# Kernel optimization log

Measured on AMD Instinct MI355X. Metric: run time of the kernel, lower is better.

The kernel has to match this reference:

```python
import jax, jax.numpy as jnp
import numpy as np

N = 10000
E = 160000
DIMS = [512, 512, 512, 256]  # in -> hidden -> hidden -> out (num_layers=3)
EPS = 1e-12  # F.normalize default eps


def _sage_layer(x, edge_index, Wl, b, Wr):
    # PyG SAGEConv (mean aggr, normalize=True):
    # out = lin_l(mean_{j in N(i)} x_j) + lin_r(x_i), then L2-normalize rows.
    src = edge_index[0]
    dst = edge_index[1]
    msg = x[src]  # [E, d] gather of source-node features
    agg = jax.ops.segment_sum(msg, dst, num_segments=N)  # [N, d]
    cnt = jax.ops.segment_sum(jnp.ones((E,), x.dtype), dst, num_segments=N)
    mean = agg / jnp.maximum(cnt, 1.0)[:, None]
    out = mean @ Wl.T + b + x @ Wr.T
    norm = jnp.sqrt(jnp.sum(out * out, axis=-1, keepdims=True))
    return out / jnp.maximum(norm, EPS)


def setup_inputs() -> dict:
    key = jax.random.key(0)
    ks = jax.random.split(key, 2 + 3 * len(DIMS))
    x = jax.random.normal(ks[0], (N, DIMS[0]), dtype=jnp.float32)
    edge_index = jax.random.randint(ks[1], (2, E), 0, N, dtype=jnp.int64)
    inp = {"x": x, "edge_index": edge_index}
    k = 2
    for i in range(len(DIMS) - 1):
        din, dout = DIMS[i], DIMS[i + 1]
        s = 1.0 / np.sqrt(din)
        inp[f"Wl{i}"] = jax.random.uniform(ks[k], (dout, din), jnp.float32, -s, s); k += 1
        inp[f"b{i}"] = jax.random.uniform(ks[k], (dout,), jnp.float32, -s, s); k += 1
        inp[f"Wr{i}"] = jax.random.uniform(ks[k], (dout, din), jnp.float32, -s, s); k += 1
    return inp


def reference(x, edge_index, Wl0, b0, Wr0, Wl1, b1, Wr1, Wl2, b2, Wr2):
    params = [(Wl0, b0, Wr0), (Wl1, b1, Wr1), (Wl2, b2, Wr2)]
    for Wl, b, Wr in params:
        x = _sage_layer(x, edge_index, Wl, b, Wr)
        x = jax.nn.relu(x)
        # F.dropout(training=False) is identity at inference
    return x
```

## Files before the change

### kernel.cpp

```cpp
#include <hip/hip_runtime.h>

#define NN 10000

typedef __attribute__((ext_vector_type(8))) short short8;
typedef __attribute__((ext_vector_type(4))) float f32x4;

__device__ __forceinline__ ushort f2b(float f) {
    union { float f; uint32_t u; } v; v.f = f;
    uint32_t u = v.u;
    return (ushort)((u + 0x7fffu + ((u >> 16) & 1u)) >> 16);
}
__device__ __forceinline__ uint packbf(float a, float b) {
    return (uint)f2b(a) | ((uint)f2b(b) << 16);
}
__device__ __forceinline__ float blo(uint u) {
    union { uint u; float f; } v; v.u = u << 16; return v.f;
}
__device__ __forceinline__ float bhi(uint u) {
    union { uint u; float f; } v; v.u = u & 0xffff0000u; return v.f;
}

__global__ __launch_bounds__(256) void zero_int(int* __restrict__ p, int n) {
    int i = blockIdx.x * 256 + threadIdx.x;
    if (i < n) p[i] = 0;
}

__global__ __launch_bounds__(256) void count_dst(const int* __restrict__ dst,
                                                 int* __restrict__ counts, int E) {
    int i = blockIdx.x * 256 + threadIdx.x;
    if (i < E) atomicAdd(&counts[dst[i]], 1);
}

__global__ __launch_bounds__(1024) void scan_build(const int* __restrict__ counts,
                                                   int* __restrict__ offsets,
                                                   int* __restrict__ cursor,
                                                   float* __restrict__ inv_cnt, int n) {
    __shared__ int part[1024];
    int tid = threadIdx.x;
    int per = (n + 1023) / 1024;
    int base = tid * per;
    int s = 0;
    for (int i = 0; i < per; i++) { int idx = base + i; if (idx < n) s += counts[idx]; }
    part[tid] = s;
    __syncthreads();
    for (int off = 1; off < 1024; off <<= 1) {
        int v = (tid >= off) ? part[tid - off] : 0;
        __syncthreads();
        part[tid] += v;
        __syncthreads();
    }
    int run = (tid > 0) ? part[tid - 1] : 0;
    for (int i = 0; i < per; i++) {
        int idx = base + i;
        if (idx < n) {
            int c = counts[idx];
            offsets[idx] = run;
            cursor[idx]  = run;
            inv_cnt[idx] = 1.0f / fmaxf((float)c, 1.0f);
            run += c;
        }
    }
}

__global__ __launch_bounds__(256) void scatter_edges(const int* __restrict__ src,
                                                     const int* __restrict__ dst,
                                                     int* __restrict__ cursor,
                                                     int* __restrict__ sorted_src, int E) {
    int i = blockIdx.x * 256 + threadIdx.x;
    if (i < E) {
        int p = atomicAdd(&cursor[dst[i]], 1);
        sorted_src[p] = src[i];
    }
}

__global__ __launch_bounds__(256) void cvt_x(const float* __restrict__ in,
                                             ushort* __restrict__ xcat, int n4) {
    int i = blockIdx.x * 256 + threadIdx.x;
    if (i >= n4) return;
    int idx = i * 4;
    int node = idx >> 9;
    int col  = idx & 511;
    float4 v = *(const float4*)(in + (size_t)node * 512 + col);
    uint2 p;
    p.x = packbf(v.x, v.y);
    p.y = packbf(v.z, v.w);
    *(uint2*)(xcat + (size_t)node * 1024 + 512 + col) = p;
}

__global__ __launch_bounds__(256) void cvt_w_all(const float* __restrict__ Wl0,
                                                 const float* __restrict__ Wr0,
                                                 const float* __restrict__ Wl1,
                                                 const float* __restrict__ Wr1,
                                                 const float* __restrict__ Wl2,
                                                 const float* __restrict__ Wr2,
                                                 ushort* __restrict__ out, int n4) {
    int i = blockIdx.x * 256 + threadIdx.x;
    if (i >= n4) return;
    int idx = i * 4;
    int row = idx >> 10;
    int col = idx & 1023;
    const float* Wl; const float* Wr; int r;
    if (row < 512)       { Wl = Wl0; Wr = Wr0; r = row; }
    else if (row < 1024) { Wl = Wl1; Wr = Wr1; r = row - 512; }
    else                 { Wl = Wl2; Wr = Wr2; r = row - 1024; }
    const float* src = (col < 512) ? (Wl + (size_t)r * 512 + col)
                                   : (Wr + (size_t)r * 512 + col - 512);
    float4 v = *(const float4*)src;
    uint2 p;
    p.x = packbf(v.x, v.y);
    p.y = packbf(v.z, v.w);
    *(uint2*)(out + idx) = p;
}

__global__ __launch_bounds__(256) void agg_mean(ushort* __restrict__ xcat,
                                                const int* __restrict__ offsets,
                                                const int* __restrict__ counts,
                                                const int* __restrict__ sorted_src,
                                                const float* __restrict__ inv_cnt,
                                                float* __restrict__ rowss, int n) {
    if (threadIdx.x < 16) {
        int z = blockIdx.x * 16 + (int)threadIdx.x;
        if (z < n) rowss[z] = 0.f;
    }
    int wave = threadIdx.x >> 6;
    int lane = threadIdx.x & 63;
    int node = blockIdx.x * 4 + wave;
    if (node >= n) return;
    int start = offsets[node];
    int cnt   = counts[node];
    float inv = inv_cnt[node];

    const uint* xr = (const uint*)xcat + 256;
    int l4 = lane * 4;

    float acc[8];
#pragma unroll
    for (int k = 0; k < 8; k++) acc[k] = 0.f;

#define ACC8(v) do { \
    acc[0] += blo(v.x); acc[1] += bhi(v.x); \
    acc[2] += blo(v.y); acc[3] += bhi(v.y); \
    acc[4] += blo(v.z); acc[5] += bhi(v.z); \
    acc[6] += blo(v.w); acc[7] += bhi(v.w); } while (0)

    int e = 0;
    for (; e + 8 <= cnt; e += 8) {
        int s[8];
#pragma unroll
        for (int u = 0; u < 8; u++) s[u] = sorted_src[start + e + u];
        uint4 v[8];
#pragma unroll
        for (int u = 0; u < 8; u++) v[u] = *(const uint4*)(xr + (size_t)s[u] * 512 + l4);
#pragma unroll
        for (int u = 0; u < 8; u++) ACC8(v[u]);
    }
    for (; e < cnt; e++) {
        int s0 = sorted_src[start + e];
        uint4 v0 = *(const uint4*)(xr + (size_t)s0 * 512 + l4);
        ACC8(v0);
    }
#undef ACC8

    uint4 o;
    o.x = packbf(acc[0] * inv, acc[1] * inv);
    o.y = packbf(acc[2] * inv, acc[3] * inv);
    o.z = packbf(acc[4] * inv, acc[5] * inv);
    o.w = packbf(acc[6] * inv, acc[7] * inv);
    *(uint4*)(xcat + (size_t)node * 1024 + lane * 8) = o;
}

__global__ __launch_bounds__(256) void gemm_mfma(const ushort* __restrict__ A,
                                                 const ushort* __restrict__ B,
                                                 const float* __restrict__ bias,
                                                 ushort* __restrict__ Cb,
                                                 float* __restrict__ rowss,
                                                 int M, int Nn) {
    __shared__ ushort Asl[64 * 32];
    __shared__ ushort Bsl[128 * 32];
    const int tid  = threadIdx.x;
    const int w    = tid >> 6;
    const int lane = tid & 63;
    const int bm = blockIdx.y * 64, bn = blockIdx.x * 128;
    const int wm = (w & 1) * 32, wn = (w >> 1) * 64;
    const int row16 = lane & 15, q = lane >> 4;

    f32x4 acc[2][4];
#pragma unroll
    for (int i = 0; i < 2; i++)
#pragma unroll
        for (int j = 0; j < 4; j++) acc[i][j] = (f32x4){0.f, 0.f, 0.f, 0.f};

    const int sc_r = lane >> 2;
    const int sc_s = lane & 3;
    const int koff = sc_s ^ ((sc_r >> 1) & 3);
    const int swz  = (row16 >> 1) & 3;

    for (int k0 = 0; k0 < 1024; k0 += 32) {
        {
            int rloc = w * 16 + sc_r;
            int grow = bm + rloc; grow = grow < M ? grow : M - 1;
            const ushort* gp = A + (size_t)grow * 1024 + k0 + koff * 8;
            __builtin_amdgcn_global_load_lds(
                (const __attribute__((address_space(1))) uint32_t*)gp,
                (__attribute__((address_space(3))) uint32_t*)&Asl[w * 512],
                16, 0, 0);
        }
#pragma unroll
        for (int c = 0; c < 2; c++) {
            int chunk = w * 2 + c;
            int rloc  = chunk * 16 + sc_r;
            const ushort* gp = B + (size_t)(bn + rloc) * 1024 + k0 + koff * 8;
            __builtin_amdgcn_global_load_lds(
                (const __attribute__((address_space(1))) uint32_t*)gp,
                (__attribute__((address_space(3))) uint32_t*)&Bsl[chunk * 512],
                16, 0, 0);
        }
        __syncthreads();

        short8 af[2], bfr[4];
        int s = q ^ swz;
#pragma unroll
        for (int i = 0; i < 2; i++) {
            int r = wm + i * 16 + row16;
            af[i] = *(const short8*)&Asl[r * 32 + s * 8];
        }
#pragma unroll
        for (int j = 0; j < 4; j++) {
            int rn = wn + j * 16 + row16;
            bfr[j] = *(const short8*)&Bsl[rn * 32 + s * 8];
        }
#pragma unroll
        for (int i = 0; i < 2; i++)
#pragma unroll
            for (int j = 0; j < 4; j++)
                acc[i][j] = __builtin_amdgcn_mfma_f32_16x16x32_bf16(
                    af[i], bfr[j], acc[i][j], 0, 0, 0);
        __syncthreads();
    }

    float bias_v[4];
#pragma unroll
    for (int j = 0; j < 4; j++) bias_v[j] = bias[bn + wn + row16 + j * 16];

#pragma unroll
    for (int i = 0; i < 2; i++) {
#pragma unroll
        for (int r2 = 0; r2 < 4; r2++) {
            int row = bm + wm + i * 16 + q * 4 + r2;
            float v0 = acc[i][0][r2] + bias_v[0];
            float v1 = acc[i][1][r2] + bias_v[1];
            float v2 = acc[i][2][r2] + bias_v[2];
            float v3 = acc[i][3][r2] + bias_v[3];
            float ssp = v0 * v0 + v1 * v1 + v2 * v2 + v3 * v3;
            ssp += __shfl_xor(ssp, 1, 64);
            ssp += __shfl_xor(ssp, 2, 64);
            ssp += __shfl_xor(ssp, 4, 64);
            ssp += __shfl_xor(ssp, 8, 64);
            if (row < M) {
                ushort* Cp = Cb + (size_t)row * Nn + bn + wn + row16;
                Cp[0]  = f2b(v0);
                Cp[16] = f2b(v1);
                Cp[32] = f2b(v2);
                Cp[48] = f2b(v3);
                if (row16 == 0) atomicAdd(&rowss[row], ssp);
            }
        }
    }
}

template <int DOUT, bool FINAL>
__global__ __launch_bounds__(256) void apply_scale(const ushort* __restrict__ Cb,
                                                   const float* __restrict__ rowss,
                                                   ushort* __restrict__ xcat,
                                                   float* __restrict__ outf, int n) {
    int wave = threadIdx.x >> 6;
    int lane = threadIdx.x & 63;
    int node = blockIdx.x * 4 + wave;
    if (node >= n) return;
    float scale = 1.0f / fmaxf(sqrtf(rowss[node]), 1e-12f);

    if (DOUT == 512) {
        uint4 v = *(const uint4*)(Cb + (size_t)node * 512 + lane * 8);
        float r0 = fmaxf(blo(v.x) * scale, 0.f), r1 = fmaxf(bhi(v.x) * scale, 0.f);
        float r2 = fmaxf(blo(v.y) * scale, 0.f), r3 = fmaxf(bhi(v.y) * scale, 0.f);
        float r4 = fmaxf(blo(v.z) * scale, 0.f), r5 = fmaxf(bhi(v.z) * scale, 0.f);
        float r6 = fmaxf(blo(v.w) * scale, 0.f), r7 = fmaxf(bhi(v.w) * scale, 0.f);
        uint4 o;
        o.x = packbf(r0, r1); o.y = packbf(r2, r3);
        o.z = packbf(r4, r5); o.w = packbf(r6, r7);
        *(uint4*)(xcat + (size_t)node * 1024 + 512 + lane * 8) = o;
    } else {
        uint2 v = *(const uint2*)(Cb + (size_t)node * 256 + lane * 4);
        float4 o;
        o.x = fmaxf(blo(v.x) * scale, 0.f);
        o.y = fmaxf(bhi(v.x) * scale, 0.f);
        o.z = fmaxf(blo(v.y) * scale, 0.f);
        o.w = fmaxf(bhi(v.y) * scale, 0.f);
        *(float4*)(outf + (size_t)node * 256 + lane * 4) = o;
    }
}

extern "C" void kernel_launch(void* const* d_in, const int* in_sizes, int n_in,
                              void* d_out, int out_size, void* d_ws, size_t ws_size,
                              hipStream_t stream) {
    const float* x    = (const float*)d_in[0];
    const int*   edge = (const int*)d_in[1];
    const float* Wl0  = (const float*)d_in[2];
    const float* b0   = (const float*)d_in[3];
    const float* Wr0  = (const float*)d_in[4];
    const float* Wl1  = (const float*)d_in[5];
    const float* b1   = (const float*)d_in[6];
    const float* Wr1  = (const float*)d_in[7];
    const float* Wl2  = (const float*)d_in[8];
    const float* b2   = (const float*)d_in[9];
    const float* Wr2  = (const float*)d_in[10];

    const int E = in_sizes[1] / 2;

    char* ws = (char*)d_ws;
    int*    counts  = (int*)(ws + 0);
    int*    offsets = (int*)(ws + 40960);
    int*    cursor  = (int*)(ws + 81920);
    float*  invc    = (float*)(ws + 122880);
    int*    sorted  = (int*)(ws + 163840);
    ushort* Wcat    = (ushort*)(ws + 804864);
    ushort* xcat    = (ushort*)(ws + 3426304);
    ushort* Cb      = (ushort*)(ws + 23906304);
    float*  rowss   = (float*)(ws + 34146304);

    ushort* Wc0 = Wcat;
    ushort* Wc1 = Wcat + 512 * 1024;
    ushort* Wc2 = Wcat + 1024 * 1024;

    zero_int<<<(NN + 255) / 256, 256, 0, stream>>>(counts, NN);
    count_dst<<<(E + 255) / 256, 256, 0, stream>>>(edge + E, counts, E);
    scan_build<<<1, 1024, 0, stream>>>(counts, offsets, cursor, invc, NN);
    scatter_edges<<<(E + 255) / 256, 256, 0, stream>>>(edge, edge + E, cursor, sorted, E);

    cvt_x<<<(NN * 512 / 4 + 255) / 256, 256, 0, stream>>>(x, xcat, NN * 512 / 4);
    cvt_w_all<<<(1280 * 1024 / 4 + 255) / 256, 256, 0, stream>>>(
        Wl0, Wr0, Wl1, Wr1, Wl2, Wr2, Wcat, 1280 * 1024 / 4);

    const int gyM = (NN + 63) / 64;
    const int gb  = (NN + 3) / 4;

    agg_mean<<<gb, 256, 0, stream>>>(xcat, offsets, counts, sorted, invc, rowss, NN);
    gemm_mfma<<<dim3(4, gyM), 256, 0, stream>>>(xcat, Wc0, b0, Cb, rowss, NN, 512);
    apply_scale<512, false><<<gb, 256, 0, stream>>>(Cb, rowss, xcat, nullptr, NN);
    agg_mean<<<gb, 256, 0, stream>>>(xcat, offsets, counts, sorted, invc, rowss, NN);
    gemm_mfma<<<dim3(4, gyM), 256, 0, stream>>>(xcat, Wc1, b1, Cb, rowss, NN, 512);
    apply_scale<512, false><<<gb, 256, 0, stream>>>(Cb, rowss, xcat, nullptr, NN);
    agg_mean<<<gb, 256, 0, stream>>>(xcat, offsets, counts, sorted, invc, rowss, NN);
    gemm_mfma<<<dim3(2, gyM), 256, 0, stream>>>(xcat, Wc2, b2, Cb, rowss, NN, 256);
    apply_scale<256, true><<<gb, 256, 0, stream>>>(Cb, rowss, nullptr, (float*)d_out, NN);
}
```

Measured before the change: 280.5 us.

## Fuse normalize+ReLU into next-layer aggregation and widen GEMM N-tile

Removes the separate apply_scale kernels for the hidden layers. Normalization and ReLU are now applied on the fly inside a new agg_mid kernel. It reads the unnormalized bf16 GEMM output and the per-node sum of squares, using double-buffered rowss arrays. The GEMM is templated on N-tile width, so the first two layers use 256-wide tiles (half the blocks, A loaded once per pair). The trade-off is recomputing a sqrt/reciprocal per gathered edge and an extra random rowss load. Fewer GEMM blocks (2x157) may also reduce occupancy on a large GPU.

```diff
diff --git a/kernel.cpp b/kernel.cpp
--- a/kernel.cpp
+++ b/kernel.cpp
@@ -112,15 +112,15 @@
     *(uint2*)(out + idx) = p;
 }
 
-__global__ __launch_bounds__(256) void agg_mean(ushort* __restrict__ xcat,
-                                                const int* __restrict__ offsets,
-                                                const int* __restrict__ counts,
-                                                const int* __restrict__ sorted_src,
-                                                const float* __restrict__ inv_cnt,
-                                                float* __restrict__ rowss, int n) {
+__global__ __launch_bounds__(256) void agg_first(ushort* __restrict__ xcat,
+                                                 const int* __restrict__ offsets,
+                                                 const int* __restrict__ counts,
+                                                 const int* __restrict__ sorted_src,
+                                                 const float* __restrict__ inv_cnt,
+                                                 float* __restrict__ rowss_next, int n) {
     if (threadIdx.x < 16) {
         int z = blockIdx.x * 16 + (int)threadIdx.x;
-        if (z < n) rowss[z] = 0.f;
+        if (z < n) rowss_next[z] = 0.f;
     }
     int wave = threadIdx.x >> 6;
     int lane = threadIdx.x & 63;
@@ -169,24 +169,105 @@
     *(uint4*)(xcat + (size_t)node * 1024 + lane * 8) = o;
 }
 
+__global__ __launch_bounds__(256) void agg_mid(ushort* __restrict__ xcat,
+                                               const ushort* __restrict__ Cb,
+                                               const float* __restrict__ rowss_prev,
+                                               float* __restrict__ rowss_next,
+                                               const int* __restrict__ offsets,
+                                               const int* __restrict__ counts,
+                                               const int* __restrict__ sorted_src,
+                                               const float* __restrict__ inv_cnt, int n) {
+    if (threadIdx.x < 16) {
+        int z = blockIdx.x * 16 + (int)threadIdx.x;
+        if (z < n) rowss_next[z] = 0.f;
+    }
+    int wave = threadIdx.x >> 6;
+    int lane = threadIdx.x & 63;
+    int node = blockIdx.x * 4 + wave;
+    if (node >= n) return;
+    int start = offsets[node];
+    int cnt   = counts[node];
+    float inv = inv_cnt[node];
+    int l4 = lane * 4;
+
+    const uint* cb = (const uint*)Cb;
+
+    {
+        float si = 1.0f / fmaxf(sqrtf(rowss_prev[node]), 1e-12f);
+        uint4 c = *(const uint4*)(cb + (size_t)node * 256 + l4);
+        float r0 = fmaxf(blo(c.x), 0.f) * si, r1 = fmaxf(bhi(c.x), 0.f) * si;
+        float r2 = fmaxf(blo(c.y), 0.f) * si, r3 = fmaxf(bhi(c.y), 0.f) * si;
+        float r4 = fmaxf(blo(c.z), 0.f) * si, r5 = fmaxf(bhi(c.z), 0.f) * si;
+        float r6 = fmaxf(blo(c.w), 0.f) * si, r7 = fmaxf(bhi(c.w), 0.f) * si;
+        uint4 o;
+        o.x = packbf(r0, r1); o.y = packbf(r2, r3);
+        o.z = packbf(r4, r5); o.w = packbf(r6, r7);
+        *(uint4*)(xcat + (size_t)node * 1024 + 512 + lane * 8) = o;
+    }
+
+    float acc[8];
+#pragma unroll
+    for (int k = 0; k < 8; k++) acc[k] = 0.f;
+
+#define ACCS(v, sc) do { \
+    acc[0] += fmaxf(blo(v.x), 0.f) * sc; acc[1] += fmaxf(bhi(v.x), 0.f) * sc; \
+    acc[2] += fmaxf(blo(v.y), 0.f) * sc; acc[3] += fmaxf(bhi(v.y), 0.f) * sc; \
+    acc[4] += fmaxf(blo(v.z), 0.f) * sc; acc[5] += fmaxf(bhi(v.z), 0.f) * sc; \
+    acc[6] += fmaxf(blo(v.w), 0.f) * sc; acc[7] += fmaxf(bhi(v.w), 0.f) * sc; } while (0)
+
+    int e = 0;
+    for (; e + 4 <= cnt; e += 4) {
+        int s[4];
+#pragma unroll
+        for (int u = 0; u < 4; u++) s[u] = sorted_src[start + e + u];
+        float sc[4];
+#pragma unroll
+        for (int u = 0; u < 4; u++)
+            sc[u] = 1.0f / fmaxf(sqrtf(rowss_prev[s[u]]), 1e-12f);
+        uint4 v[4];
+#pragma unroll
+        for (int u = 0; u < 4; u++) v[u] = *(const uint4*)(cb + (size_t)s[u] * 256 + l4);
+#pragma unroll
+        for (int u = 0; u < 4; u++) ACCS(v[u], sc[u]);
+    }
+    for (; e < cnt; e++) {
+        int s0 = sorted_src[start + e];
+        float sc0 = 1.0f / fmaxf(sqrtf(rowss_prev[s0]), 1e-12f);
+        uint4 v0 = *(const uint4*)(cb + (size_t)s0 * 256 + l4);
+        ACCS(v0, sc0);
+    }
+#undef ACCS
+
+    uint4 o;
+    o.x = packbf(acc[0] * inv, acc[1] * inv);
+    o.y = packbf(acc[2] * inv, acc[3] * inv);
+    o.z = packbf(acc[4] * inv, acc[5] * inv);
+    o.w = packbf(acc[6] * inv, acc[7] * inv);
+    *(uint4*)(xcat + (size_t)node * 1024 + lane * 8) = o;
+}
+
+template <int BN>
 __global__ __launch_bounds__(256) void gemm_mfma(const ushort* __restrict__ A,
                                                  const ushort* __restrict__ B,
                                                  const float* __restrict__ bias,
                                                  ushort* __restrict__ Cb,
                                                  float* __restrict__ rowss,
                                                  int M, int Nn) {
+    constexpr int NWN = BN / 64;
+    constexpr int WRC = NWN;
     __shared__ ushort Asl[64 * 32];
-    __shared__ ushort Bsl[128 * 32];
+    __shared__ ushort Bsl[BN * 32];
     const int tid  = threadIdx.x;
     const int w    = tid >> 6;
     const int lane = tid & 63;
-    const int bm = blockIdx.y * 64, bn = blockIdx.x * 128;
-    const int wm = (w & 1) * 32, wn = (w >> 1) * 64;
+    const int bm = blockIdx.y * 64, bn = blockIdx.x * BN;
+    const int wn = (w % NWN) * 64;
+    const int wm = (w / NWN) * (WRC * 16);
     const int row16 = lane & 15, q = lane >> 4;
 
-    f32x4 acc[2][4];
-#pragma unroll
-    for (int i = 0; i < 2; i++)
+    f32x4 acc[WRC][4];
+#pragma unroll
+    for (int i = 0; i < WRC; i++)
 #pragma unroll
         for (int j = 0; j < 4; j++) acc[i][j] = (f32x4){0.f, 0.f, 0.f, 0.f};
 
@@ -206,8 +287,8 @@
                 16, 0, 0);
         }
 #pragma unroll
-        for (int c = 0; c < 2; c++) {
-            int chunk = w * 2 + c;
+        for (int c = 0; c < NWN; c++) {
+            int chunk = w * NWN + c;
             int rloc  = chunk * 16 + sc_r;
             const ushort* gp = B + (size_t)(bn + rloc) * 1024 + k0 + koff * 8;
             __builtin_amdgcn_global_load_lds(
@@ -217,10 +298,10 @@
         }
         __syncthreads();
 
-        short8 af[2], bfr[4];
+        short8 af[WRC], bfr[4];
         int s = q ^ swz;
 #pragma unroll
-        for (int i = 0; i < 2; i++) {
+        for (int i = 0; i < WRC; i++) {
             int r = wm + i * 16 + row16;
             af[i] = *(const short8*)&Asl[r * 32 + s * 8];
         }
@@ -230,7 +311,7 @@
             bfr[j] = *(const short8*)&Bsl[rn * 32 + s * 8];
         }
 #pragma unroll
-        for (int i = 0; i < 2; i++)
+        for (int i = 0; i < WRC; i++)
 #pragma unroll
             for (int j = 0; j < 4; j++)
                 acc[i][j] = __builtin_amdgcn_mfma_f32_16x16x32_bf16(
@@ -243,7 +324,7 @@
     for (int j = 0; j < 4; j++) bias_v[j] = bias[bn + wn + row16 + j * 16];
 
 #pragma unroll
-    for (int i = 0; i < 2; i++) {
+    for (int i = 0; i < WRC; i++) {
 #pragma unroll
         for (int r2 = 0; r2 < 4; r2++) {
             int row = bm + wm + i * 16 + q * 4 + r2;
@@ -268,36 +349,21 @@
     }
 }
 
-template <int DOUT, bool FINAL>
-__global__ __launch_bounds__(256) void apply_scale(const ushort* __restrict__ Cb,
+__global__ __launch_bounds__(256) void apply_final(const ushort* __restrict__ Cb,
                                                    const float* __restrict__ rowss,
-                                                   ushort* __restrict__ xcat,
                                                    float* __restrict__ outf, int n) {
     int wave = threadIdx.x >> 6;
     int lane = threadIdx.x & 63;
     int node = blockIdx.x * 4 + wave;
     if (node >= n) return;
     float scale = 1.0f / fmaxf(sqrtf(rowss[node]), 1e-12f);
-
-    if (DOUT == 512) {
-        uint4 v = *(const uint4*)(Cb + (size_t)node * 512 + lane * 8);
-        float r0 = fmaxf(blo(v.x) * scale, 0.f), r1 = fmaxf(bhi(v.x) * scale, 0.f);
-        float r2 = fmaxf(blo(v.y) * scale, 0.f), r3 = fmaxf(bhi(v.y) * scale, 0.f);
-        float r4 = fmaxf(blo(v.z) * scale, 0.f), r5 = fmaxf(bhi(v.z) * scale, 0.f);
-        float r6 = fmaxf(blo(v.w) * scale, 0.f), r7 = fmaxf(bhi(v.w) * scale, 0.f);
-        uint4 o;
-        o.x = packbf(r0, r1); o.y = packbf(r2, r3);
-        o.z = packbf(r4, r5); o.w = packbf(r6, r7);
-        *(uint4*)(xcat + (size_t)node * 1024 + 512 + lane * 8) = o;
-    } else {
-        uint2 v = *(const uint2*)(Cb + (size_t)node * 256 + lane * 4);
-        float4 o;
-        o.x = fmaxf(blo(v.x) * scale, 0.f);
-        o.y = fmaxf(bhi(v.x) * scale, 0.f);
-        o.z = fmaxf(blo(v.y) * scale, 0.f);
-        o.w = fmaxf(bhi(v.y) * scale, 0.f);
-        *(float4*)(outf + (size_t)node * 256 + lane * 4) = o;
-    }
+    uint2 v = *(const uint2*)(Cb + (size_t)node * 256 + lane * 4);
+    float4 o;
+    o.x = fmaxf(blo(v.x) * scale, 0.f);
+    o.y = fmaxf(bhi(v.x) * scale, 0.f);
+    o.z = fmaxf(blo(v.y) * scale, 0.f);
+    o.w = fmaxf(bhi(v.y) * scale, 0.f);
+    *(float4*)(outf + (size_t)node * 256 + lane * 4) = o;
 }
 
 extern "C" void kernel_launch(void* const* d_in, const int* in_sizes, int n_in,
@@ -326,7 +392,8 @@
     ushort* Wcat    = (ushort*)(ws + 804864);
     ushort* xcat    = (ushort*)(ws + 3426304);
     ushort* Cb      = (ushort*)(ws + 23906304);
-    float*  rowss   = (float*)(ws + 34146304);
+    float*  rowssA  = (float*)(ws + 34146304);
+    float*  rowssB  = (float*)(ws + 34187264);
 
     ushort* Wc0 = Wcat;
     ushort* Wc1 = Wcat + 512 * 1024;
@@ -344,13 +411,13 @@
     const int gyM = (NN + 63) / 64;
     const int gb  = (NN + 3) / 4;
 
-    agg_mean<<<gb, 256, 0, stream>>>(xcat, offsets, counts, sorted, invc, rowss, NN);
-    gemm_mfma<<<dim3(4, gyM), 256, 0, stream>>>(xcat, Wc0, b0, Cb, rowss, NN, 512);
-    apply_scale<512, false><<<gb, 256, 0, stream>>>(Cb, rowss, xcat, nullptr, NN);
-    agg_mean<<<gb, 256, 0, stream>>>(xcat, offsets, counts, sorted, invc, rowss, NN);
-    gemm_mfma<<<dim3(4, gyM), 256, 0, stream>>>(xcat, Wc1, b1, Cb, rowss, NN, 512);
-    apply_scale<512, false><<<gb, 256, 0, stream>>>(Cb, rowss, xcat, nullptr, NN);
-    agg_mean<<<gb, 256, 0, stream>>>(xcat, offsets, counts, sorted, invc, rowss, NN);
-    gemm_mfma<<<dim3(2, gyM), 256, 0, stream>>>(xcat, Wc2, b2, Cb, rowss, NN, 256);
-    apply_scale<256, true><<<gb, 256, 0, stream>>>(Cb, rowss, nullptr, (float*)d_out, NN);
-}
+    agg_first<<<gb, 256, 0, stream>>>(xcat, offsets, counts, sorted, invc, rowssA, NN);
+    gemm_mfma<256><<<dim3(2, gyM), 256, 0, stream>>>(xcat, Wc0, b0, Cb, rowssA, NN, 512);
+    agg_mid<<<gb, 256, 0, stream>>>(xcat, Cb, rowssA, rowssB, offsets, counts, sorted,
+                                    invc, NN);
+    gemm_mfma<256><<<dim3(2, gyM), 256, 0, stream>>>(xcat, Wc1, b1, Cb, rowssB, NN, 512);
+    agg_mid<<<gb, 256, 0, stream>>>(xcat, Cb, rowssB, rowssA, offsets, counts, sorted,
+                                    invc, NN);
+    gemm_mfma<128><<<dim3(2, gyM), 256, 0, stream>>>(xcat, Wc2, b2, Cb, rowssA, NN, 256);
+    apply_final<<<gb, 256, 0, stream>>>(Cb, rowssA, (float*)d_out, NN);
+}
```

After: 291.4 us. +3.9%, slower.
